# Kernel optimization log

Measured on AMD Instinct MI355X. Metric: run time of the kernel, lower is better.

## Reference

```python
import jax, jax.numpy as jnp
import numpy as np

B, S, D, H = 2, 2048, 1024, 16
DK = D // H  # 64


def _quantum(x, W1, b1, W2, b2):
    # Stand-in for QuantumNeuralLayer: classical->quantum->classical, d_k -> d_k.
    return jnp.tanh(x @ W1 + b1) @ W2 + b2


def setup_inputs() -> dict:
    key = jax.random.key(0)
    ks = jax.random.split(key, 16)
    s = 1.0 / np.sqrt(DK)
    inp = {
        "q": jax.random.normal(ks[0], (B, S, D), dtype=jnp.float32),
        "k": jax.random.normal(ks[1], (B, S, D), dtype=jnp.float32),
        "v": jax.random.normal(ks[2], (B, S, D), dtype=jnp.float32),
    }
    names = ["q", "k", "v"]
    for i, n in enumerate(names):
        inp[f"W{n}1"] = jax.random.normal(ks[3 + 4 * i], (DK, DK), dtype=jnp.float32) * s
        inp[f"b{n}1"] = jnp.zeros((DK,), dtype=jnp.float32)
        inp[f"W{n}2"] = jax.random.normal(ks[4 + 4 * i], (DK, DK), dtype=jnp.float32) * s
        inp[f"b{n}2"] = jnp.zeros((DK,), dtype=jnp.float32)
    inp["Wo"] = jax.random.normal(ks[15], (D, D), dtype=jnp.float32) * (1.0 / np.sqrt(D))
    inp["bo"] = jnp.zeros((D,), dtype=jnp.float32)
    return inp


def reference(q, k, v, Wq1, bq1, Wq2, bq2, Wk1, bk1, Wk2, bk2,
              Wv1, bv1, Wv2, bv2, Wo, bo):
    b, s, _ = q.shape
    # split heads: [B, S, H, DK]
    qh = q.reshape(b, s, H, DK)
    kh = k.reshape(b, s, H, DK)
    vh = v.reshape(b, s, H, DK)
    # quantum per-feature transform on last dim
    qh = _quantum(qh, Wq1, bq1, Wq2, bq2)
    kh = _quantum(kh, Wk1, bk1, Wk2, bk2)
    vh = _quantum(vh, Wv1, bv1, Wv2, bv2)
    scale = 1.0 / jnp.sqrt(jnp.asarray(DK, dtype=qh.dtype))
    # scores: [B, H, S, S]
    scores = jnp.einsum("bqhd,bkhd->bhqk", qh, kh) * scale
    attn = jax.nn.softmax(scores, axis=-1)
    # context: [B, H, S, DK] -> [B, S, D]
    ctx = jnp.einsum("bhqk,bkhd->bqhd", attn, vh).reshape(b, s, D)
    return ctx @ Wo + bo
```

## Files before the change

kernel.cpp:

```cpp
#include <hip/hip_runtime.h>

#define B_ 2
#define S_ 2048
#define D_ 1024
#define H_ 16
#define DK_ 64

typedef float f32x4 __attribute__((ext_vector_type(4)));
typedef float f32x16 __attribute__((ext_vector_type(16)));
typedef short bf16x8 __attribute__((ext_vector_type(8)));

static __device__ __forceinline__ unsigned short f2bf(float f) {
  unsigned u = __float_as_uint(f);
  unsigned r = (u + 0x7FFFu + ((u >> 16) & 1u)) >> 16;
  return (unsigned short)r;
}

static __device__ __forceinline__ unsigned cvtpk_bf16(float lo, float hi) {
  unsigned r;
  asm("v_cvt_pk_bf16_f32 %0, %1, %2" : "=v"(r) : "v"(lo), "v"(hi));
  return r;
}

static __device__ __forceinline__ void load16_lds(const void* g, void* lds) {
  __builtin_amdgcn_global_load_lds(
      (const __attribute__((address_space(1))) unsigned int*)g,
      (__attribute__((address_space(3))) unsigned int*)lds, 16, 0, 0);
}

static __device__ __forceinline__ bf16x8 make_pa8(const float* p, int hi) {
  unsigned x1 = cvtpk_bf16(p[0], p[1]);
  unsigned x2 = cvtpk_bf16(p[2], p[3]);
  unsigned y1 = cvtpk_bf16(p[4], p[5]);
  unsigned y2 = cvtpk_bf16(p[6], p[7]);
  asm("v_permlane32_swap_b32 %0, %1" : "+v"(x1), "+v"(y1));
  asm("v_permlane32_swap_b32 %0, %1" : "+v"(x2), "+v"(y2));
  union {
    unsigned u[4];
    bf16x8 v;
  } pa;
  pa.u[0] = x1;
  pa.u[1] = x2;
  pa.u[2] = y1;
  pa.u[3] = y2;
  (void)hi;
  return pa.v;
}

static __device__ __forceinline__ float tanh_fast(float x) {
  float xc = fminf(fmaxf(x, -9.0f), 9.0f);
  float e = exp2f(xc * 2.88539008177792681472f);
  return (e - 1.0f) / (e + 1.0f);
}

__global__ __launch_bounds__(256) void quantum_fused(
    const float* __restrict__ xq, const float* __restrict__ xk,
    const float* __restrict__ xv,
    const float* __restrict__ Wq1, const float* __restrict__ bq1,
    const float* __restrict__ Wq2, const float* __restrict__ bq2,
    const float* __restrict__ Wk1, const float* __restrict__ bk1,
    const float* __restrict__ Wk2, const float* __restrict__ bk2,
    const float* __restrict__ Wv1, const float* __restrict__ bv1,
    const float* __restrict__ Wv2, const float* __restrict__ bv2,
    const float* __restrict__ Wo, unsigned short* __restrict__ WoT,
    unsigned short* __restrict__ qhb, unsigned short* __restrict__ khb,
    unsigned short* __restrict__ vtb, float qscale) {
  __shared__ float tt[64][65];

  const int tid = threadIdx.x;

  if (blockIdx.z == 3) {
    if (blockIdx.y >= 16) return;
    const int k0 = blockIdx.x * 64, n0 = blockIdx.y * 64;
    const int r = tid >> 4, c4 = tid & 15;
#pragma unroll
    for (int i = 0; i < 4; ++i) {
      float4 v = *(const float4*)&Wo[(size_t)(k0 + r + 16 * i) * D_ + n0 + c4 * 4];
      tt[r + 16 * i][c4 * 4 + 0] = v.x;
      tt[r + 16 * i][c4 * 4 + 1] = v.y;
      tt[r + 16 * i][c4 * 4 + 2] = v.z;
      tt[r + 16 * i][c4 * 4 + 3] = v.w;
    }
    __syncthreads();
    const int n = tid >> 2, kc = tid & 3;
    union {
      unsigned short u[16];
      uint4 v[2];
    } pk;
#pragma unroll
    for (int j = 0; j < 16; ++j) pk.u[j] = f2bf(tt[kc * 16 + j][n]);
    unsigned short* op = WoT + (size_t)(n0 + n) * D_ + k0 + kc * 16;
    *(uint4*)op = pk.v[0];
    *(uint4*)(op + 8) = pk.v[1];
    return;
  }

  const int w = tid >> 6;
  const int l = tid & 63;
  const int lq = l & 31;
  const int hi = l >> 5;
  const int bh = blockIdx.y;
  const int b = bh >> 4, h = bh & 15;
  const int s0w = blockIdx.x * 128 + w * 32;

  const float* x;
  const float* W1;
  const float* b1;
  const float* W2;
  const float* b2;
  unsigned short* outp;
  float scale = 1.0f;
  int vmode = 0;
  if (blockIdx.z == 0) {
    x = xq; W1 = Wq1; b1 = bq1; W2 = Wq2; b2 = bq2; outp = qhb;
    scale = qscale;
  } else if (blockIdx.z == 1) {
    x = xk; W1 = Wk1; b1 = bk1; W2 = Wk2; b2 = bk2; outp = khb;
  } else {
    x = xv; W1 = Wv1; b1 = bv1; W2 = Wv2; b2 = bv2; outp = vtb;
    vmode = 1;
  }

  bf16x8 w1f[2][4];
#pragma unroll
  for (int ca = 0; ca < 2; ++ca)
#pragma unroll
    for (int kc = 0; kc < 4; ++kc) {
      const float* wp = W1 + (size_t)(kc * 16 + hi * 8) * 64 + ca * 32 + lq;
      union {
        unsigned u[4];
        bf16x8 v;
      } ww;
#pragma unroll
      for (int jj = 0; jj < 4; ++jj)
        ww.u[jj] = cvtpk_bf16(wp[(2 * jj) * 64], wp[(2 * jj + 1) * 64]);
      w1f[ca][kc] = ww.v;
    }

  const float* xrow = x + (((size_t)b * S_ + s0w + lq) * H_ + h) * DK_;
  bf16x8 xf[4];
#pragma unroll
  for (int kc = 0; kc < 4; ++kc) {
    float4 f0 = *(const float4*)(xrow + kc * 16 + hi * 8);
    float4 f1 = *(const float4*)(xrow + kc * 16 + hi * 8 + 4);
    union {
      unsigned u[4];
      bf16x8 v;
    } xx;
    xx.u[0] = cvtpk_bf16(f0.x, f0.y);
    xx.u[1] = cvtpk_bf16(f0.z, f0.w);
    xx.u[2] = cvtpk_bf16(f1.x, f1.y);
    xx.u[3] = cvtpk_bf16(f1.z, f1.w);
    xf[kc] = xx.v;
  }

  f32x16 acc1[2];
#pragma unroll
  for (int ca = 0; ca < 2; ++ca)
#pragma unroll
    for (int r = 0; r < 16; ++r)
      acc1[ca][r] = b1[ca * 32 + (r & 3) + 8 * (r >> 2) + 4 * hi];
#pragma unroll
  for (int kc = 0; kc < 4; ++kc) {
    acc1[0] = __builtin_amdgcn_mfma_f32_32x32x16_bf16(w1f[0][kc], xf[kc], acc1[0], 0, 0, 0);
    acc1[1] = __builtin_amdgcn_mfma_f32_32x32x16_bf16(w1f[1][kc], xf[kc], acc1[1], 0, 0, 0);
  }

  float t0[16], t1[16];
#pragma unroll
  for (int r = 0; r < 16; ++r) {
    t0[r] = tanh_fast(acc1[0][r]);
    t1[r] = tanh_fast(acc1[1][r]);
  }

  bf16x8 af[4];
  af[0] = make_pa8(&t0[0], hi);
  af[1] = make_pa8(&t0[8], hi);
  af[2] = make_pa8(&t1[0], hi);
  af[3] = make_pa8(&t1[8], hi);

  bf16x8 w2f[2][4];
#pragma unroll
  for (int nb = 0; nb < 2; ++nb)
#pragma unroll
    for (int kc = 0; kc < 4; ++kc) {
      const float* wp = W2 + (size_t)(kc * 16 + hi * 8) * 64 + nb * 32 + lq;
      union {
        unsigned u[4];
        bf16x8 v;
      } ww;
#pragma unroll
      for (int jj = 0; jj < 4; ++jj)
        ww.u[jj] = cvtpk_bf16(wp[(2 * jj) * 64], wp[(2 * jj + 1) * 64]);
      w2f[nb][kc] = ww.v;
    }

  f32x16 acc2[2];
#pragma unroll
  for (int nb = 0; nb < 2; ++nb)
#pragma unroll
    for (int r = 0; r < 16; ++r)
      acc2[nb][r] = b2[nb * 32 + (r & 3) + 8 * (r >> 2) + 4 * hi];
#pragma unroll
  for (int kc = 0; kc < 4; ++kc) {
    acc2[0] = __builtin_amdgcn_mfma_f32_32x32x16_bf16(af[kc], w2f[0][kc], acc2[0], 0, 0, 0);
    acc2[1] = __builtin_amdgcn_mfma_f32_32x32x16_bf16(af[kc], w2f[1][kc], acc2[1], 0, 0, 0);
  }

  if (!vmode) {
#pragma unroll
    for (int nb = 0; nb < 2; ++nb)
#pragma unroll
      for (int r = 0; r < 16; ++r) {
        const int s = s0w + (r & 3) + 8 * (r >> 2) + 4 * hi;
        outp[((size_t)bh * S_ + s) * DK_ + nb * 32 + lq] =
            f2bf(acc2[nb][r] * scale);
      }
  } else {
#pragma unroll
    for (int nb = 0; nb < 2; ++nb) {
      float yv[16];
#pragma unroll
      for (int r = 0; r < 16; ++r) yv[r] = acc2[nb][r];
      const size_t rowb = ((size_t)bh * DK_ + nb * 32 + lq) * S_;
      *(bf16x8*)(outp + rowb + s0w + hi * 8) = make_pa8(&yv[0], hi);
      *(bf16x8*)(outp + rowb + s0w + 16 + hi * 8) = make_pa8(&yv[8], hi);
    }
  }
}

__global__ __launch_bounds__(512, 2) void attn_kernel(
    const unsigned short* __restrict__ qhb,
    const unsigned short* __restrict__ khb,
    const unsigned short* __restrict__ vtb,
    unsigned short* __restrict__ ctxb) {
  __shared__ __align__(16) unsigned short kvbuf[2][2][64 * 64];

  const int tid = threadIdx.x;
  const int w = tid >> 6;
  const int l = tid & 63;
  const int lq = l & 31;
  const int hi = l >> 5;
  const int bh = blockIdx.x;
  const int b = bh >> 4, h = bh & 15;
  const int q0 = blockIdx.y * 256 + w * 32;

  const unsigned short* qp = qhb + ((size_t)bh * S_ + q0 + lq) * DK_ + hi * 8;
  bf16x8 qf[4];
#pragma unroll
  for (int kc = 0; kc < 4; ++kc) qf[kc] = *(const bf16x8*)(qp + kc * 16);

  f32x16 o0 = {}, o1 = {};
  f32x16 lacc = {};

  union {
    unsigned u[4];
    bf16x8 v;
  } onesu;
  onesu.u[0] = 0x3F803F80u;
  onesu.u[1] = 0x3F803F80u;
  onesu.u[2] = 0x3F803F80u;
  onesu.u[3] = 0x3F803F80u;
  const bf16x8 ones = onesu.v;

  const unsigned short* kgbase = khb + (size_t)bh * S_ * DK_;
  const unsigned short* vgbase = vtb + (size_t)bh * DK_ * S_;
  const int srow = tid >> 3;
  const int sl8 = ((tid & 7) ^ (srow & 7)) * 8;

  const unsigned short* kp = kgbase + (size_t)srow * DK_ + sl8;
  const unsigned short* vp = vgbase + (size_t)srow * S_ + sl8;

#define STAGE(BUF)                                                            \
  {                                                                           \
    load16_lds(kp, (char*)kvbuf[BUF][0] + w * 1024);                          \
    load16_lds(vp, (char*)kvbuf[BUF][1] + w * 1024);                          \
    kp += 64 * DK_;                                                           \
    vp += 64;                                                                 \
  }

  STAGE(0)
  __syncthreads();

  for (int t = 0; t < 32; ++t) {
    const int cur = t & 1;
    const char* ksP = (const char*)kvbuf[cur][0];
    const char* vsP = (const char*)kvbuf[cur][1];
    if (t < 31) STAGE(cur ^ 1)

    f32x16 s0a = {}, s0b = {};
    __builtin_amdgcn_s_setprio(1);
#pragma unroll
    for (int kc = 0; kc < 4; ++kc) {
      const int so = ((kc * 2 + hi) ^ (lq & 7)) << 4;
      bf16x8 ka = *(const bf16x8*)(ksP + lq * 128 + so);
      bf16x8 kb = *(const bf16x8*)(ksP + (32 + lq) * 128 + so);
      s0a = __builtin_amdgcn_mfma_f32_32x32x16_bf16(ka, qf[kc], s0a, 0, 0, 0);
      s0b = __builtin_amdgcn_mfma_f32_32x32x16_bf16(kb, qf[kc], s0b, 0, 0, 0);
    }
    __builtin_amdgcn_s_setprio(0);

#pragma unroll
    for (int i = 0; i < 16; ++i) s0a[i] = exp2f(s0a[i]);
#pragma unroll
    for (int i = 0; i < 16; ++i) s0b[i] = exp2f(s0b[i]);

    float pv[8];
    __builtin_amdgcn_s_setprio(1);
#pragma unroll
    for (int kc = 0; kc < 4; ++kc) {
#pragma unroll
      for (int j = 0; j < 8; ++j) pv[j] = (kc < 2) ? s0a[(kc & 1) * 8 + j]
                                                   : s0b[(kc & 1) * 8 + j];
      bf16x8 pav = make_pa8(pv, hi);
      const int slot = kc * 2 + hi;
      bf16x8 v0 = *(const bf16x8*)(vsP + lq * 128 + ((slot ^ (lq & 7)) << 4));
      bf16x8 v1 = *(const bf16x8*)(vsP + (32 + lq) * 128 + ((slot ^ (lq & 7)) << 4));
      o0 = __builtin_amdgcn_mfma_f32_32x32x16_bf16(pav, v0, o0, 0, 0, 0);
      o1 = __builtin_amdgcn_mfma_f32_32x32x16_bf16(pav, v1, o1, 0, 0, 0);
      lacc = __builtin_amdgcn_mfma_f32_32x32x16_bf16(pav, ones, lacc, 0, 0, 0);
    }
    __builtin_amdgcn_s_setprio(0);

    __syncthreads();
  }
#undef STAGE

#pragma unroll
  for (int r = 0; r < 16; ++r) {
    const int crow = ((r & 3) + 8 * (r >> 2)) + 4 * hi;
    const float li = 1.0f / lacc[r];
    const int qg = q0 + crow;
    const size_t base = ((size_t)b * S_ + qg) * D_ + h * DK_;
    ctxb[base + lq] = f2bf(o0[r] * li);
    ctxb[base + 32 + lq] = f2bf(o1[r] * li);
  }
}

__global__ __launch_bounds__(256) void out_gemm_mfma(
    const unsigned short* __restrict__ A,
    const unsigned short* __restrict__ BT,
    const float* __restrict__ bo, float* __restrict__ C) {
  __shared__ __align__(16) unsigned short As[3][128 * 64];
  __shared__ __align__(16) unsigned short Bs[3][128 * 64];

  const int tid = threadIdx.x;
  const int w = tid >> 6, l = tid & 63;
  const int ll = l & 15, lg = l >> 4;
  const int wr = w >> 1, wc = w & 1;
  const int m0 = blockIdx.y * 128, n0 = blockIdx.x * 128;

  const int srow = l >> 3;
  const int sslot = (l & 7) ^ srow;
  const int g_off = sslot * 8;

  f32x4 acc[4][4];
#pragma unroll
  for (int mt = 0; mt < 4; ++mt)
#pragma unroll
    for (int nt = 0; nt < 4; ++nt) acc[mt][nt] = (f32x4){0.f, 0.f, 0.f, 0.f};

#define STAGE_G(BUF, KT)                                                      \
  {                                                                           \
    const int k0e = (KT)*64;                                                  \
    _Pragma("unroll") for (int c = 0; c < 4; ++c) {                           \
      const int row = c * 32 + w * 8 + srow;                                  \
      load16_lds(A + (size_t)(m0 + row) * D_ + k0e + g_off,                   \
                 (char*)As[BUF] + c * 4096 + w * 1024);                       \
      load16_lds(BT + (size_t)(n0 + row) * D_ + k0e + g_off,                  \
                 (char*)Bs[BUF] + c * 4096 + w * 1024);                       \
    }                                                                         \
  }

  STAGE_G(0, 0)
  STAGE_G(1, 1)

  for (int kt = 0; kt < 16; ++kt) {
    if (kt < 15) {
      asm volatile("s_waitcnt vmcnt(8)" ::: "memory");
    } else {
      asm volatile("s_waitcnt vmcnt(0)" ::: "memory");
    }
    __builtin_amdgcn_sched_barrier(0);
    __builtin_amdgcn_s_barrier();
    __builtin_amdgcn_sched_barrier(0);

    const int cur = kt % 3;
    if (kt < 14) STAGE_G((kt + 2) % 3, kt + 2)

#pragma unroll
    for (int half = 0; half < 2; ++half) {
      bf16x8 af[4], bfr[4];
#pragma unroll
      for (int mt = 0; mt < 4; ++mt) {
        const int row = wr * 64 + mt * 16 + ll;
        af[mt] = *(const bf16x8*)((const char*)As[cur] + row * 128 +
                                  (((half * 4 + lg) ^ (row & 7)) << 4));
      }
#pragma unroll
      for (int nt = 0; nt < 4; ++nt) {
        const int rowb = wc * 64 + nt * 16 + ll;
        bfr[nt] = *(const bf16x8*)((const char*)Bs[cur] + rowb * 128 +
                                   (((half * 4 + lg) ^ (rowb & 7)) << 4));
      }
      __builtin_amdgcn_s_setprio(1);
#pragma unroll
      for (int mt = 0; mt < 4; ++mt)
#pragma unroll
        for (int nt = 0; nt < 4; ++nt)
          acc[mt][nt] = __builtin_amdgcn_mfma_f32_16x16x32_bf16(
              af[mt], bfr[nt], acc[mt][nt], 0, 0, 0);
      __builtin_amdgcn_s_setprio(0);
    }
  }
#undef STAGE_G

#pragma unroll
  for (int nt = 0; nt < 4; ++nt) {
    const int col = n0 + wc * 64 + nt * 16 + ll;
    const float bv = bo[col];
#pragma unroll
    for (int mt = 0; mt < 4; ++mt) {
      const int row0 = m0 + wr * 64 + mt * 16 + lg * 4;
#pragma unroll
      for (int r = 0; r < 4; ++r)
        C[(size_t)(row0 + r) * D_ + col] = acc[mt][nt][r] + bv;
    }
  }
}

extern "C" void kernel_launch(void* const* d_in, const int* in_sizes, int n_in,
                              void* d_out, int out_size, void* d_ws,
                              size_t ws_size, hipStream_t stream) {
  const float* q = (const float*)d_in[0];
  const float* k = (const float*)d_in[1];
  const float* v = (const float*)d_in[2];
  const float* Wq1 = (const float*)d_in[3];
  const float* bq1 = (const float*)d_in[4];
  const float* Wq2 = (const float*)d_in[5];
  const float* bq2 = (const float*)d_in[6];
  const float* Wk1 = (const float*)d_in[7];
  const float* bk1 = (const float*)d_in[8];
  const float* Wk2 = (const float*)d_in[9];
  const float* bk2 = (const float*)d_in[10];
  const float* Wv1 = (const float*)d_in[11];
  const float* bv1 = (const float*)d_in[12];
  const float* Wv2 = (const float*)d_in[13];
  const float* bv2 = (const float*)d_in[14];
  const float* Wo = (const float*)d_in[15];
  const float* bo = (const float*)d_in[16];
  float* out = (float*)d_out;

  const size_t TEN = (size_t)B_ * H_ * S_ * DK_;
  char* ws = (char*)d_ws;
  unsigned short* qhb = (unsigned short*)ws;
  unsigned short* khb = (unsigned short*)(ws + TEN * 2);
  unsigned short* vtb = (unsigned short*)(ws + TEN * 4);
  unsigned short* ctxb = (unsigned short*)(ws + TEN * 6);
  unsigned short* wot = (unsigned short*)(ws + TEN * 8);

  const float cs = 0.125f * 1.44269504088896340736f;
  quantum_fused<<<dim3(16, 32, 4), 256, 0, stream>>>(
      q, k, v, Wq1, bq1, Wq2, bq2, Wk1, bk1, Wk2, bk2, Wv1, bv1, Wv2, bv2,
      Wo, wot, qhb, khb, vtb, cs);

  attn_kernel<<<dim3(32, 8), 512, 0, stream>>>(qhb, khb, vtb, ctxb);

  out_gemm_mfma<<<dim3(8, 32), 256, 0, stream>>>(ctxb, wot, bo, out);
}
```

Before: 100.2 us.

## Drop LDS staging in attention; load K/V directly from global per wave

Replaces the 8-wave block that double-buffered K and V tiles through shared memory with single-wave blocks that read K and V fragments straight from global memory each iteration. This removes the block-wide barriers, the LDS staging and the priority hints, and launches eight times as many blocks. In exchange, each K/V tile is now fetched once per wave rather than once per block, so global and L2 traffic rises, and load latency is no longer hidden by prefetching.

```diff
diff --git a/kernel.cpp b/kernel.cpp
--- a/kernel.cpp
+++ b/kernel.cpp
@@ -229,21 +229,17 @@
   }
 }
 
-__global__ __launch_bounds__(512, 2) void attn_kernel(
+__global__ __launch_bounds__(64) void attn_kernel(
     const unsigned short* __restrict__ qhb,
     const unsigned short* __restrict__ khb,
     const unsigned short* __restrict__ vtb,
     unsigned short* __restrict__ ctxb) {
-  __shared__ __align__(16) unsigned short kvbuf[2][2][64 * 64];
-
-  const int tid = threadIdx.x;
-  const int w = tid >> 6;
-  const int l = tid & 63;
+  const int l = threadIdx.x;
   const int lq = l & 31;
   const int hi = l >> 5;
   const int bh = blockIdx.x;
   const int b = bh >> 4, h = bh & 15;
-  const int q0 = blockIdx.y * 256 + w * 32;
+  const int q0 = blockIdx.y * 32;
 
   const unsigned short* qp = qhb + ((size_t)bh * S_ + q0 + lq) * DK_ + hi * 8;
   bf16x8 qf[4];
@@ -263,42 +259,22 @@
   onesu.u[3] = 0x3F803F80u;
   const bf16x8 ones = onesu.v;
 
-  const unsigned short* kgbase = khb + (size_t)bh * S_ * DK_;
-  const unsigned short* vgbase = vtb + (size_t)bh * DK_ * S_;
-  const int srow = tid >> 3;
-  const int sl8 = ((tid & 7) ^ (srow & 7)) * 8;
-
-  const unsigned short* kp = kgbase + (size_t)srow * DK_ + sl8;
-  const unsigned short* vp = vgbase + (size_t)srow * S_ + sl8;
-
-#define STAGE(BUF)                                                            \
-  {                                                                           \
-    load16_lds(kp, (char*)kvbuf[BUF][0] + w * 1024);                          \
-    load16_lds(vp, (char*)kvbuf[BUF][1] + w * 1024);                          \
-    kp += 64 * DK_;                                                           \
-    vp += 64;                                                                 \
-  }
-
-  STAGE(0)
-  __syncthreads();
+  const unsigned short* ka_p = khb + ((size_t)bh * S_ + lq) * DK_ + hi * 8;
+  const unsigned short* kb_p = ka_p + 32 * DK_;
+  const unsigned short* va_p = vtb + ((size_t)bh * DK_ + lq) * S_ + hi * 8;
+  const unsigned short* vb_p = va_p + 32 * S_;
 
   for (int t = 0; t < 32; ++t) {
-    const int cur = t & 1;
-    const char* ksP = (const char*)kvbuf[cur][0];
-    const char* vsP = (const char*)kvbuf[cur][1];
-    if (t < 31) STAGE(cur ^ 1)
-
     f32x16 s0a = {}, s0b = {};
-    __builtin_amdgcn_s_setprio(1);
 #pragma unroll
     for (int kc = 0; kc < 4; ++kc) {
-      const int so = ((kc * 2 + hi) ^ (lq & 7)) << 4;
-      bf16x8 ka = *(const bf16x8*)(ksP + lq * 128 + so);
-      bf16x8 kb = *(const bf16x8*)(ksP + (32 + lq) * 128 + so);
+      bf16x8 ka = *(const bf16x8*)(ka_p + kc * 16);
+      bf16x8 kb = *(const bf16x8*)(kb_p + kc * 16);
       s0a = __builtin_amdgcn_mfma_f32_32x32x16_bf16(ka, qf[kc], s0a, 0, 0, 0);
       s0b = __builtin_amdgcn_mfma_f32_32x32x16_bf16(kb, qf[kc], s0b, 0, 0, 0);
     }
-    __builtin_amdgcn_s_setprio(0);
+    ka_p += 64 * DK_;
+    kb_p += 64 * DK_;
 
 #pragma unroll
     for (int i = 0; i < 16; ++i) s0a[i] = exp2f(s0a[i]);
@@ -306,25 +282,21 @@
     for (int i = 0; i < 16; ++i) s0b[i] = exp2f(s0b[i]);
 
     float pv[8];
-    __builtin_amdgcn_s_setprio(1);
 #pragma unroll
     for (int kc = 0; kc < 4; ++kc) {
 #pragma unroll
       for (int j = 0; j < 8; ++j) pv[j] = (kc < 2) ? s0a[(kc & 1) * 8 + j]
                                                    : s0b[(kc & 1) * 8 + j];
       bf16x8 pav = make_pa8(pv, hi);
-      const int slot = kc * 2 + hi;
-      bf16x8 v0 = *(const bf16x8*)(vsP + lq * 128 + ((slot ^ (lq & 7)) << 4));
-      bf16x8 v1 = *(const bf16x8*)(vsP + (32 + lq) * 128 + ((slot ^ (lq & 7)) << 4));
+      bf16x8 v0 = *(const bf16x8*)(va_p + kc * 16);
+      bf16x8 v1 = *(const bf16x8*)(vb_p + kc * 16);
       o0 = __builtin_amdgcn_mfma_f32_32x32x16_bf16(pav, v0, o0, 0, 0, 0);
       o1 = __builtin_amdgcn_mfma_f32_32x32x16_bf16(pav, v1, o1, 0, 0, 0);
       lacc = __builtin_amdgcn_mfma_f32_32x32x16_bf16(pav, ones, lacc, 0, 0, 0);
     }
-    __builtin_amdgcn_s_setprio(0);
-
-    __syncthreads();
-  }
-#undef STAGE
+    va_p += 64;
+    vb_p += 64;
+  }
 
 #pragma unroll
   for (int r = 0; r < 16; ++r) {
@@ -464,7 +436,7 @@
       q, k, v, Wq1, bq1, Wq2, bq2, Wk1, bk1, Wk2, bk2, Wv1, bv1, Wv2, bv2,
       Wo, wot, qhb, khb, vtb, cs);
 
-  attn_kernel<<<dim3(32, 8), 512, 0, stream>>>(qhb, khb, vtb, ctxb);
+  attn_kernel<<<dim3(32, 64), 64, 0, stream>>>(qhb, khb, vtb, ctxb);
 
   out_gemm_mfma<<<dim3(8, 32), 256, 0, stream>>>(ctxb, wot, bo, out);
 }
```

Measured after the change: 164.2 us. 63.9% more time.

## Shrink output GEMM tile to 128x64 with double-buffered LDS pipeline

Applied to the files above, without the earlier changes.

The output projection GEMM now uses 128x64 tiles instead of 128x128, which doubles the grid to 512 blocks so more of the CUs are busy. It also replaces the 3-stage LDS ring with manual vmcnt waits by a simpler 2-stage double buffer synchronised with __syncthreads. In exchange, each block reuses loaded data less, and the prefetch distance drops to one stage with a full barrier every iteration.

```diff
diff --git a/kernel.cpp b/kernel.cpp
--- a/kernel.cpp
+++ b/kernel.cpp
@@ -341,87 +341,81 @@
     const unsigned short* __restrict__ A,
     const unsigned short* __restrict__ BT,
     const float* __restrict__ bo, float* __restrict__ C) {
-  __shared__ __align__(16) unsigned short As[3][128 * 64];
-  __shared__ __align__(16) unsigned short Bs[3][128 * 64];
+  __shared__ __align__(16) unsigned short As[2][128 * 64];
+  __shared__ __align__(16) unsigned short Bs[2][64 * 64];
 
   const int tid = threadIdx.x;
   const int w = tid >> 6, l = tid & 63;
   const int ll = l & 15, lg = l >> 4;
-  const int wr = w >> 1, wc = w & 1;
-  const int m0 = blockIdx.y * 128, n0 = blockIdx.x * 128;
+  const int m0 = blockIdx.y * 128, n0 = blockIdx.x * 64;
 
   const int srow = l >> 3;
-  const int sslot = (l & 7) ^ srow;
-  const int g_off = sslot * 8;
-
-  f32x4 acc[4][4];
-#pragma unroll
-  for (int mt = 0; mt < 4; ++mt)
+  const int sl8 = ((l & 7) ^ srow) * 8;
+
+  f32x4 acc[2][4];
+#pragma unroll
+  for (int mt = 0; mt < 2; ++mt)
 #pragma unroll
     for (int nt = 0; nt < 4; ++nt) acc[mt][nt] = (f32x4){0.f, 0.f, 0.f, 0.f};
 
 #define STAGE_G(BUF, KT)                                                      \
   {                                                                           \
     const int k0e = (KT)*64;                                                  \
-    _Pragma("unroll") for (int c = 0; c < 4; ++c) {                           \
-      const int row = c * 32 + w * 8 + srow;                                  \
-      load16_lds(A + (size_t)(m0 + row) * D_ + k0e + g_off,                   \
-                 (char*)As[BUF] + c * 4096 + w * 1024);                       \
-      load16_lds(BT + (size_t)(n0 + row) * D_ + k0e + g_off,                  \
-                 (char*)Bs[BUF] + c * 4096 + w * 1024);                       \
+    _Pragma("unroll") for (int j = 0; j < 4; ++j) {                           \
+      const int rowa = (w * 4 + j) * 8 + srow;                                \
+      load16_lds(A + (size_t)(m0 + rowa) * D_ + k0e + sl8,                    \
+                 (char*)As[BUF] + (w * 4 + j) * 1024);                        \
     }                                                                         \
+    _Pragma("unroll") for (int j = 0; j < 2; ++j) {                           \
+      const int rowb = (w * 2 + j) * 8 + srow;                                \
+      load16_lds(BT + (size_t)(n0 + rowb) * D_ + k0e + sl8,                   \
+                 (char*)Bs[BUF] + (w * 2 + j) * 1024);                        \
+    }                                                                         \
   }
 
   STAGE_G(0, 0)
-  STAGE_G(1, 1)
+  __syncthreads();
 
   for (int kt = 0; kt < 16; ++kt) {
-    if (kt < 15) {
-      asm volatile("s_waitcnt vmcnt(8)" ::: "memory");
-    } else {
-      asm volatile("s_waitcnt vmcnt(0)" ::: "memory");
-    }
-    __builtin_amdgcn_sched_barrier(0);
-    __builtin_amdgcn_s_barrier();
-    __builtin_amdgcn_sched_barrier(0);
-
-    const int cur = kt % 3;
-    if (kt < 14) STAGE_G((kt + 2) % 3, kt + 2)
+    const int cur = kt & 1;
+    if (kt < 15) STAGE_G(cur ^ 1, kt + 1)
 
 #pragma unroll
     for (int half = 0; half < 2; ++half) {
-      bf16x8 af[4], bfr[4];
-#pragma unroll
-      for (int mt = 0; mt < 4; ++mt) {
-        const int row = wr * 64 + mt * 16 + ll;
+      bf16x8 af[2], bfr[4];
+#pragma unroll
+      for (int mt = 0; mt < 2; ++mt) {
+        const int row = w * 32 + mt * 16 + ll;
         af[mt] = *(const bf16x8*)((const char*)As[cur] + row * 128 +
                                   (((half * 4 + lg) ^ (row & 7)) << 4));
       }
 #pragma unroll
       for (int nt = 0; nt < 4; ++nt) {
-        const int rowb = wc * 64 + nt * 16 + ll;
+        const int rowb = nt * 16 + ll;
         bfr[nt] = *(const bf16x8*)((const char*)Bs[cur] + rowb * 128 +
                                    (((half * 4 + lg) ^ (rowb & 7)) << 4));
       }
       __builtin_amdgcn_s_setprio(1);
 #pragma unroll
-      for (int mt = 0; mt < 4; ++mt)
+      for (int mt = 0; mt < 2; ++mt)
 #pragma unroll
         for (int nt = 0; nt < 4; ++nt)
           acc[mt][nt] = __builtin_amdgcn_mfma_f32_16x16x32_bf16(
               af[mt], bfr[nt], acc[mt][nt], 0, 0, 0);
       __builtin_amdgcn_s_setprio(0);
     }
+
+    __syncthreads();
   }
 #undef STAGE_G
 
 #pragma unroll
   for (int nt = 0; nt < 4; ++nt) {
-    const int col = n0 + wc * 64 + nt * 16 + ll;
+    const int col = n0 + nt * 16 + ll;
     const float bv = bo[col];
 #pragma unroll
-    for (int mt = 0; mt < 4; ++mt) {
-      const int row0 = m0 + wr * 64 + mt * 16 + lg * 4;
+    for (int mt = 0; mt < 2; ++mt) {
+      const int row0 = m0 + w * 32 + mt * 16 + lg * 4;
 #pragma unroll
       for (int r = 0; r < 4; ++r)
         C[(size_t)(row0 + r) * D_ + col] = acc[mt][nt][r] + bv;
@@ -466,5 +460,5 @@
 
   attn_kernel<<<dim3(32, 8), 512, 0, stream>>>(qhb, khb, vtb, ctxb);
 
-  out_gemm_mfma<<<dim3(8, 32), 256, 0, stream>>>(ctxb, wot, bo, out);
-}
+  out_gemm_mfma<<<dim3(16, 32), 256, 0, stream>>>(ctxb, wot, bo, out);
+}
```

Measured after the change: 98.73 us. About the same (-1.5%).
